# Performance work log

Hardware: AMD Instinct MI355X
Metric: run time of the kernel (lower is better)

The kernel has to match this reference:

```python
import jax, jax.numpy as jnp
import numpy as np

N = 50000        # num_nodes
E = 1_600_000    # num_edges
C = 64           # out_channels
P = 10           # periods (window_size)


def _glorot(k, shape):
    lim = np.sqrt(6.0 / (shape[0] + shape[1]))
    return jax.random.uniform(k, shape, jnp.float32, -lim, lim)


def setup_inputs() -> dict:
    key = jax.random.key(0)
    ks = jax.random.split(key, 12)
    x = jax.random.normal(ks[0], (N, 1, P), jnp.float32)
    edge_index = jax.random.randint(ks[1], (2, E), 0, N, dtype=jnp.int64)
    inp = {
        "x": x,
        "edge_index": edge_index,
        # GCNConv weights/biases for the 3 gates (in_channels=1 -> C)
        "w_cz": _glorot(ks[2], (1, C)), "b_cz": jnp.zeros((C,), jnp.float32),
        "w_cr": _glorot(ks[3], (1, C)), "b_cr": jnp.zeros((C,), jnp.float32),
        "w_ch": _glorot(ks[4], (1, C)), "b_ch": jnp.zeros((C,), jnp.float32),
        # GRU gate linears: Linear(2C -> C), stored as [in, out]
        "w_lz": _glorot(ks[5], (2 * C, C)), "b_lz": jnp.zeros((C,), jnp.float32),
        "w_lr": _glorot(ks[6], (2 * C, C)), "b_lr": jnp.zeros((C,), jnp.float32),
        "w_lh": _glorot(ks[7], (2 * C, C)), "b_lh": jnp.zeros((C,), jnp.float32),
        # temporal attention logits over periods
        "attention": jax.random.uniform(ks[8], (P,), jnp.float32),
        # output head Linear(C -> 1)
        "w_out": _glorot(ks[9], (C, 1)), "b_out": jnp.zeros((1,), jnp.float32),
    }
    return inp


def reference(x, edge_index, w_cz, b_cz, w_cr, b_cr, w_ch, b_ch,
              w_lz, b_lz, w_lr, b_lr, w_lh, b_lh, attention, w_out, b_out):
    # --- GCN symmetric normalization with self-loops (computed once) ---
    row, col = edge_index[0], edge_index[1]
    loop = jnp.arange(N, dtype=row.dtype)
    row_f = jnp.concatenate([row, loop])
    col_f = jnp.concatenate([col, loop])
    ones = jnp.ones(E + N, jnp.float32)
    deg = jax.ops.segment_sum(ones, col_f, num_segments=N)
    dinv = jnp.where(deg > 0, jax.lax.rsqrt(deg), 0.0)
    norm = dinv[row_f] * dinv[col_f]                       # [E+N]

    def gcn(xt, W, b):
        # xt: [N,1] -> lin -> propagate D^-1/2 (A+I) D^-1/2 -> + bias
        h = xt @ W                                          # [N,C]
        msg = h[row_f] * norm[:, None]                      # [E+N,C]
        return jax.ops.segment_sum(msg, col_f, num_segments=N) + b

    probs = jax.nn.softmax(attention)                       # [P]
    xs = jnp.transpose(x, (2, 0, 1))                        # [P,N,1]

    def step(carry, inp):
        H, Hacc = carry
        xt, p = inp
        Z = jax.nn.sigmoid(jnp.concatenate([gcn(xt, w_cz, b_cz), H], 1) @ w_lz + b_lz)
        R = jax.nn.sigmoid(jnp.concatenate([gcn(xt, w_cr, b_cr), H], 1) @ w_lr + b_lr)
        Ht = jnp.tanh(jnp.concatenate([gcn(xt, w_ch, b_ch), H * R], 1) @ w_lh + b_lh)
        Hn = Z * H + (1.0 - Z) * Ht
        return (Hn, Hacc + p * Hn), None

    H0 = jnp.zeros((N, C), jnp.float32)
    (_, Hacc), _ = jax.lax.scan(step, (H0, H0), (xs, probs))

    out = jnp.maximum(Hacc, 0.0) @ w_out + b_out            # ReLU + Linear(C->1)
    return out.squeeze(-1)                                   # [N]
```

## Files before the change

### kernel.cpp

```cpp
#include <hip/hip_runtime.h>
#include <math.h>


#define PT 10
#define PS 12
#define CC 64
#define CAP 96

__global__ void k_zero(unsigned int* p, int n) {
  int i = blockIdx.x * 256 + threadIdx.x;
  if (i < n) p[i] = 0u;
}

__global__ void k_deg(const int* __restrict__ col, unsigned int* deg, int E) {
  int e = blockIdx.x * 256 + threadIdx.x;
  if (e < E) atomicAdd(&deg[col[e]], 1u);
}

__global__ void k_scan1(const unsigned int* __restrict__ deg, unsigned int* rowstart,
                        unsigned int* blocksum, int n) {
  __shared__ unsigned int tmp[256];
  int i = blockIdx.x * 256 + threadIdx.x;
  unsigned int v = (i < n) ? deg[i] : 0u;
  tmp[threadIdx.x] = v;
  __syncthreads();
  for (int off = 1; off < 256; off <<= 1) {
    unsigned int t = (threadIdx.x >= off) ? tmp[threadIdx.x - off] : 0u;
    __syncthreads();
    tmp[threadIdx.x] += t;
    __syncthreads();
  }
  if (i < n) rowstart[i] = tmp[threadIdx.x] - v;
  if (threadIdx.x == 255) blocksum[blockIdx.x] = tmp[255];
}

__global__ void k_scan2(unsigned int* bs, int nb) {
  __shared__ unsigned int tmp[256];
  unsigned int v = (threadIdx.x < nb) ? bs[threadIdx.x] : 0u;
  tmp[threadIdx.x] = v;
  __syncthreads();
  for (int off = 1; off < 256; off <<= 1) {
    unsigned int t = (threadIdx.x >= off) ? tmp[threadIdx.x - off] : 0u;
    __syncthreads();
    tmp[threadIdx.x] += t;
    __syncthreads();
  }
  if (threadIdx.x < nb) bs[threadIdx.x] = tmp[threadIdx.x] - v;
}

__global__ void k_scan3(unsigned int* rowstart, const unsigned int* __restrict__ bs,
                        unsigned int* cursor, int n) {
  int i = blockIdx.x * 256 + threadIdx.x;
  if (i < n) {
    unsigned int v = rowstart[i] + bs[blockIdx.x];
    rowstart[i] = v;
    cursor[i] = v;
  }
}

__global__ void k_dinv_y(const unsigned int* __restrict__ deg, const float* __restrict__ x,
                         float* __restrict__ dinv, float* __restrict__ y, int n) {
  int v = blockIdx.x * 256 + threadIdx.x;
  if (v >= n) return;
  float di = rsqrtf((float)(deg[v] + 1u));
  dinv[v] = di;
  float* yr = y + (size_t)v * PS;
  const float* xr = x + (size_t)v * PT;
#pragma unroll
  for (int t = 0; t < PT; ++t) yr[t] = di * xr[t];
  yr[10] = 0.0f;
  yr[11] = 0.0f;
}

__global__ void k_scatter(const int* __restrict__ row, const int* __restrict__ col,
                          unsigned int* cnt_or_cursor, unsigned int* __restrict__ csr,
                          int E, int cap) {
  int e = blockIdx.x * 256 + threadIdx.x;
  if (e >= E) return;
  int c = col[e];
  unsigned int slot = atomicAdd(&cnt_or_cursor[c], 1u);
  if (cap > 0) {
    if (slot < (unsigned int)cap) csr[(size_t)c * cap + slot] = (unsigned int)row[e];
  } else {
    csr[slot] = (unsigned int)row[e];
  }
}

__global__ __launch_bounds__(256) void k_gather(
    const unsigned int* __restrict__ csr, const unsigned int* __restrict__ starts,
    const unsigned int* __restrict__ counts, const float* __restrict__ y,
    const float* __restrict__ dinv, float* __restrict__ s, int n, int cap) {
  int tid = blockIdx.x * 256 + threadIdx.x;
  int v = tid >> 2, l = tid & 3;
  if (v >= n) return;
  unsigned int cnt = counts[v];
  unsigned int start;
  if (cap > 0) {
    start = (unsigned int)v * (unsigned int)cap;
    if (cnt > (unsigned int)cap) cnt = (unsigned int)cap;
  } else {
    start = starts[v];
  }
  float a[PS];
#pragma unroll
  for (int t = 0; t < PS; ++t) a[t] = 0.0f;
  unsigned int end = start + cnt;
  for (unsigned int e = start + (unsigned int)l; e < end; e += 4u) {
    unsigned int r = csr[e];
    const float4* yr = (const float4*)(y + (size_t)r * PS);
    float4 b0 = yr[0], b1 = yr[1], b2 = yr[2];
    a[0] += b0.x; a[1] += b0.y; a[2] += b0.z; a[3] += b0.w;
    a[4] += b1.x; a[5] += b1.y; a[6] += b1.z; a[7] += b1.w;
    a[8] += b2.x; a[9] += b2.y; a[10] += b2.z; a[11] += b2.w;
  }
#pragma unroll
  for (int m = 1; m < 4; m <<= 1) {
#pragma unroll
    for (int t = 0; t < PS; ++t) a[t] += __shfl_xor(a[t], m, 64);
  }
  if (l == 0) {
    float di = dinv[v];
    const float4* ys = (const float4*)(y + (size_t)v * PS);
    float4 b0 = ys[0], b1 = ys[1], b2 = ys[2];
    float4 o0, o1, o2;
    o0.x = di * (a[0] + b0.x); o0.y = di * (a[1] + b0.y);
    o0.z = di * (a[2] + b0.z); o0.w = di * (a[3] + b0.w);
    o1.x = di * (a[4] + b1.x); o1.y = di * (a[5] + b1.y);
    o1.z = di * (a[6] + b1.z); o1.w = di * (a[7] + b1.w);
    o2.x = di * (a[8] + b2.x); o2.y = di * (a[9] + b2.y);
    o2.z = di * (a[10] + b2.z); o2.w = di * (a[11] + b2.w);
    float4* sv = (float4*)(s + (size_t)v * PS);
    sv[0] = o0; sv[1] = o1; sv[2] = o2;
  }
}

__global__ void k_sinit_fb(const float* __restrict__ y, const float* __restrict__ dinv,
                           float* __restrict__ s, int n) {
  int v = blockIdx.x * 256 + threadIdx.x;
  if (v >= n) return;
  float di = dinv[v];
#pragma unroll
  for (int t = 0; t < PS; ++t) s[(size_t)v * PS + t] = di * y[(size_t)v * PS + t];
}

__global__ void k_edge_fb(const int* __restrict__ row, const int* __restrict__ col,
                          const float* __restrict__ dinv, const float* __restrict__ y,
                          float* __restrict__ s, int E) {
  int e = blockIdx.x * 256 + threadIdx.x;
  if (e >= E) return;
  int r = row[e], c = col[e];
  float dc = dinv[c];
  const float* yr = y + (size_t)r * PS;
  float* sc = s + (size_t)c * PS;
#pragma unroll
  for (int t = 0; t < PT; ++t) atomicAdd(&sc[t], dc * yr[t]);
}

__global__ void k_prep(const float* wcz, const float* bcz, const float* wcr, const float* bcr,
                       const float* wch, const float* bch,
                       const float* wlz, const float* blz, const float* wlr, const float* blr,
                       const float* wlh, const float* blh, float* coef) {
  int c = threadIdx.x;
  float az = 0, ar = 0, ah = 0, bz = 0, br = 0, bh = 0;
  for (int m = 0; m < CC; ++m) {
    float z = wlz[m * CC + c], r = wlr[m * CC + c], h = wlh[m * CC + c];
    az += wcz[m] * z;  ar += wcr[m] * r;  ah += wch[m] * h;
    bz += bcz[m] * z;  br += bcr[m] * r;  bh += bch[m] * h;
  }
  coef[0 * CC + c] = az;
  coef[1 * CC + c] = ar;
  coef[2 * CC + c] = ah;
  coef[3 * CC + c] = bz + blz[c];
  coef[4 * CC + c] = br + blr[c];
  coef[5 * CC + c] = bh + blh[c];
}

__device__ __forceinline__ float sigf(float v) { return 1.0f / (1.0f + __expf(-v)); }
__device__ __forceinline__ float tanhfastf(float v) { return 2.0f / (1.0f + __expf(-2.0f * v)) - 1.0f; }

__device__ __forceinline__ int swz(int r, int ch) { return (ch ^ ((r >> 2) & 7)) << 2; }

__global__ __launch_bounds__(256, 4) void k_gru(
    const float* __restrict__ s, const float* __restrict__ coef,
    const float* __restrict__ wlz, const float* __restrict__ wlr, const float* __restrict__ wlh,
    const float* __restrict__ attention, const float* __restrict__ w_out,
    const float* __restrict__ b_out, float* __restrict__ out, int n) {
  __shared__ float HT[64][64];
  __shared__ float QT[64][64];
  __shared__ float sT[64][12];

  const int tid = threadIdx.x;
  const int i = tid >> 5;
  const int j = tid & 31;
  const int n0 = blockIdx.x * 64;

  for (int idx = tid; idx < 64 * 64; idx += 256) ((float*)HT)[idx] = 0.0f;
  for (int idx = tid; idx < 64 * PT; idx += 256) {
    int nn = idx / PT, t = idx - nn * PT;
    int g = n0 + nn;
    sT[nn][t] = (g < n) ? s[(size_t)g * PS + t] : 0.0f;
  }

  float att[PT];
#pragma unroll
  for (int t = 0; t < PT; ++t) att[t] = attention[t];
  float mx = att[0];
#pragma unroll
  for (int t = 1; t < PT; ++t) mx = fmaxf(mx, att[t]);
  float ssum = 0.0f;
#pragma unroll
  for (int t = 0; t < PT; ++t) { att[t] = __expf(att[t] - mx); ssum += att[t]; }
  float sinv = 1.0f / ssum;
#pragma unroll
  for (int t = 0; t < PT; ++t) att[t] *= sinv;

  const int c2 = 2 * j;
  const float2 aZ = *(const float2*)(coef + 0 + c2);
  const float2 aR = *(const float2*)(coef + 64 + c2);
  const float2 aH = *(const float2*)(coef + 128 + c2);
  const float2 bZ = *(const float2*)(coef + 192 + c2);
  const float2 bR = *(const float2*)(coef + 256 + c2);
  const float2 bH = *(const float2*)(coef + 320 + c2);
  const float* WZ = wlz + 64 * CC + c2;
  const float* WR = wlr + 64 * CC + c2;
  const float* WH = wlh + 64 * CC + c2;
  const float2 wo2 = *(const float2*)(w_out + c2);

  float hacc[8][2];
#pragma unroll
  for (int nn = 0; nn < 8; ++nn) { hacc[nn][0] = 0.0f; hacc[nn][1] = 0.0f; }

  __syncthreads();

  for (int t = 0; t < PT; ++t) {
    float sloc[8];
#pragma unroll
    for (int nn = 0; nn < 8; ++nn) sloc[nn] = sT[8 * i + nn][t];

    float acc[8][4];
#pragma unroll
    for (int nn = 0; nn < 8; ++nn) {
      acc[nn][0] = fmaf(sloc[nn], aZ.x, bZ.x);
      acc[nn][1] = fmaf(sloc[nn], aZ.y, bZ.y);
      acc[nn][2] = fmaf(sloc[nn], aR.x, bR.x);
      acc[nn][3] = fmaf(sloc[nn], aR.y, bR.y);
    }
#pragma unroll 4
    for (int k = 0; k < 64; ++k) {
      const float2 wz = *(const float2*)(WZ + (k << 6));
      const float2 wr = *(const float2*)(WR + (k << 6));
      const float4 h0 = *(const float4*)&HT[k][swz(k, 2 * i)];
      const float4 h1 = *(const float4*)&HT[k][swz(k, 2 * i + 1)];
      const float hh[8] = {h0.x, h0.y, h0.z, h0.w, h1.x, h1.y, h1.z, h1.w};
#pragma unroll
      for (int nn = 0; nn < 8; ++nn) {
        acc[nn][0] = fmaf(hh[nn], wz.x, acc[nn][0]);
        acc[nn][1] = fmaf(hh[nn], wz.y, acc[nn][1]);
        acc[nn][2] = fmaf(hh[nn], wr.x, acc[nn][2]);
        acc[nn][3] = fmaf(hh[nn], wr.y, acc[nn][3]);
      }
    }

    float hold[2][8], zreg[2][8];
#pragma unroll
    for (int cc = 0; cc < 2; ++cc) {
      int r = c2 + cc;
      float4 h0 = *(const float4*)&HT[r][swz(r, 2 * i)];
      float4 h1 = *(const float4*)&HT[r][swz(r, 2 * i + 1)];
      hold[cc][0] = h0.x; hold[cc][1] = h0.y; hold[cc][2] = h0.z; hold[cc][3] = h0.w;
      hold[cc][4] = h1.x; hold[cc][5] = h1.y; hold[cc][6] = h1.z; hold[cc][7] = h1.w;
      float4 q0, q1;
      q0.x = hold[cc][0] * sigf(acc[0][2 + cc]); q0.y = hold[cc][1] * sigf(acc[1][2 + cc]);
      q0.z = hold[cc][2] * sigf(acc[2][2 + cc]); q0.w = hold[cc][3] * sigf(acc[3][2 + cc]);
      q1.x = hold[cc][4] * sigf(acc[4][2 + cc]); q1.y = hold[cc][5] * sigf(acc[5][2 + cc]);
      q1.z = hold[cc][6] * sigf(acc[6][2 + cc]); q1.w = hold[cc][7] * sigf(acc[7][2 + cc]);
      *(float4*)&QT[r][swz(r, 2 * i)] = q0;
      *(float4*)&QT[r][swz(r, 2 * i + 1)] = q1;
#pragma unroll
      for (int nn = 0; nn < 8; ++nn) zreg[cc][nn] = sigf(acc[nn][cc]);
    }
    __syncthreads();

    float acc2[8][2];
#pragma unroll
    for (int nn = 0; nn < 8; ++nn) {
      acc2[nn][0] = fmaf(sloc[nn], aH.x, bH.x);
      acc2[nn][1] = fmaf(sloc[nn], aH.y, bH.y);
    }
#pragma unroll 4
    for (int k = 0; k < 64; ++k) {
      const float2 wv = *(const float2*)(WH + (k << 6));
      const float4 q0 = *(const float4*)&QT[k][swz(k, 2 * i)];
      const float4 q1 = *(const float4*)&QT[k][swz(k, 2 * i + 1)];
      const float qq[8] = {q0.x, q0.y, q0.z, q0.w, q1.x, q1.y, q1.z, q1.w};
#pragma unroll
      for (int nn = 0; nn < 8; ++nn) {
        acc2[nn][0] = fmaf(qq[nn], wv.x, acc2[nn][0]);
        acc2[nn][1] = fmaf(qq[nn], wv.y, acc2[nn][1]);
      }
    }

#pragma unroll
    for (int cc = 0; cc < 2; ++cc) {
      int r = c2 + cc;
      float hn[8];
#pragma unroll
      for (int nn = 0; nn < 8; ++nn) {
        float ht = tanhfastf(acc2[nn][cc]);
        float z = zreg[cc][nn];
        float v = z * hold[cc][nn] + (1.0f - z) * ht;
        hn[nn] = v;
        hacc[nn][cc] = fmaf(att[t], v, hacc[nn][cc]);
      }
      float4 v0 = make_float4(hn[0], hn[1], hn[2], hn[3]);
      float4 v1 = make_float4(hn[4], hn[5], hn[6], hn[7]);
      *(float4*)&HT[r][swz(r, 2 * i)] = v0;
      *(float4*)&HT[r][swz(r, 2 * i + 1)] = v1;
    }
    __syncthreads();
  }

  float p[8];
#pragma unroll
  for (int nn = 0; nn < 8; ++nn)
    p[nn] = fmaxf(hacc[nn][0], 0.0f) * wo2.x + fmaxf(hacc[nn][1], 0.0f) * wo2.y;
#pragma unroll
  for (int m = 1; m < 32; m <<= 1) {
#pragma unroll
    for (int nn = 0; nn < 8; ++nn) p[nn] += __shfl_xor(p[nn], m, 64);
  }
  if (j == 0) {
    float bo = b_out[0];
#pragma unroll
    for (int nn = 0; nn < 8; ++nn) {
      int g = n0 + 8 * i + nn;
      if (g < n) out[g] = p[nn] + bo;
    }
  }
}

extern "C" void kernel_launch(void* const* d_in, const int* in_sizes, int n_in,
                              void* d_out, int out_size, void* d_ws, size_t ws_size,
                              hipStream_t stream) {
  const float* x    = (const float*)d_in[0];
  const int*   ei   = (const int*)d_in[1];
  const float* wcz  = (const float*)d_in[2];
  const float* bcz  = (const float*)d_in[3];
  const float* wcr  = (const float*)d_in[4];
  const float* bcr  = (const float*)d_in[5];
  const float* wch  = (const float*)d_in[6];
  const float* bch  = (const float*)d_in[7];
  const float* wlz  = (const float*)d_in[8];
  const float* blz  = (const float*)d_in[9];
  const float* wlr  = (const float*)d_in[10];
  const float* blr  = (const float*)d_in[11];
  const float* wlh  = (const float*)d_in[12];
  const float* blh  = (const float*)d_in[13];
  const float* att  = (const float*)d_in[14];
  const float* wout = (const float*)d_in[15];
  const float* bout = (const float*)d_in[16];
  float* out = (float*)d_out;

  const int N = out_size;
  const int E = in_sizes[1] / 2;
  const int* row = ei;
  const int* col = ei + E;

  char* ws = (char*)d_ws;
  size_t off = 0;
  auto alloc = [&](size_t bytes) {
    char* p = ws + off;
    off += (bytes + 15) & ~15ull;
    return p;
  };
  unsigned int* cnt  = (unsigned int*)alloc((size_t)N * 4);
  float*        dinv = (float*)alloc((size_t)N * 4);
  float*        y    = (float*)alloc((size_t)N * PS * 4);
  float*        s    = (float*)alloc((size_t)N * PS * 4);
  float*        coef = (float*)alloc(384 * 4);
  size_t commonEnd = off;

  const size_t needA = commonEnd + (size_t)N * CAP * 4;
  const size_t needB = commonEnd + (size_t)N * 8 + 256 * 4 + (size_t)E * 4 + 64;

  const int nbN = (N + 255) / 256;
  const int nbE = (E + 255) / 256;

  k_prep<<<1, 64, 0, stream>>>(wcz, bcz, wcr, bcr, wch, bch, wlz, blz, wlr, blr, wlh, blh, coef);

  if (ws_size >= needA) {
    unsigned int* csr = (unsigned int*)(ws + commonEnd);
    k_zero<<<nbN, 256, 0, stream>>>(cnt, N);
    k_scatter<<<nbE, 256, 0, stream>>>(row, col, cnt, csr, E, CAP);
    k_dinv_y<<<nbN, 256, 0, stream>>>(cnt, x, dinv, y, N);
    k_gather<<<(4 * N + 255) / 256, 256, 0, stream>>>(csr, nullptr, cnt, y, dinv, s, N, CAP);
  } else if (ws_size >= needB) {
    size_t o = commonEnd;
    unsigned int* rowstart = (unsigned int*)(ws + o); o += (size_t)N * 4;
    unsigned int* cursor   = (unsigned int*)(ws + o); o += (size_t)N * 4;
    unsigned int* blocksum = (unsigned int*)(ws + o); o += 256 * 4;
    unsigned int* csr      = (unsigned int*)(ws + o);
    k_zero<<<nbN, 256, 0, stream>>>(cnt, N);
    k_deg<<<nbE, 256, 0, stream>>>(col, cnt, E);
    k_scan1<<<nbN, 256, 0, stream>>>(cnt, rowstart, blocksum, N);
    k_scan2<<<1, 256, 0, stream>>>(blocksum, nbN);
    k_scan3<<<nbN, 256, 0, stream>>>(rowstart, blocksum, cursor, N);
    k_dinv_y<<<nbN, 256, 0, stream>>>(cnt, x, dinv, y, N);
    k_scatter<<<nbE, 256, 0, stream>>>(row, col, cursor, csr, E, 0);
    k_gather<<<(4 * N + 255) / 256, 256, 0, stream>>>(csr, rowstart, cnt, y, dinv, s, N, 0);
  } else {
    k_zero<<<nbN, 256, 0, stream>>>(cnt, N);
    k_deg<<<nbE, 256, 0, stream>>>(col, cnt, E);
    k_dinv_y<<<nbN, 256, 0, stream>>>(cnt, x, dinv, y, N);
    k_sinit_fb<<<nbN, 256, 0, stream>>>(y, dinv, s, N);
    k_edge_fb<<<nbE, 256, 0, stream>>>(row, col, dinv, y, s, E);
  }

  k_gru<<<(N + 63) / 64, 256, 0, stream>>>(s, coef, wlz, wlr, wlh, att, wout, bout, out, N);
}
```

Before: 551.5 us.

## Halve GRU node tile to 32 and pack Z/R weights into float4

The GRU kernel now processes 32 nodes per block instead of 64, with half-size shared tiles, fewer accumulators per thread, a new swizzle, and launch bounds raised to 8 blocks per SM for higher occupancy and more blocks. The prep kernel also interleaves the hidden-part Z and R weight columns into a float4 array so each k step needs one vector global load instead of two. The trade-off is that every weight load is now reused across only 4 nodes instead of 8, which doubles total weight traffic and the number of loop iterations per node.

```diff
diff --git a/kernel.cpp b/kernel.cpp
--- a/kernel.cpp
+++ b/kernel.cpp
@@ -5,6 +5,7 @@
 #define PT 10
 #define PS 12
 #define CC 64
+#define NB 32
 #define CAP 96
 
 __global__ void k_zero(unsigned int* p, int n) {
@@ -159,43 +160,52 @@
 __global__ void k_prep(const float* wcz, const float* bcz, const float* wcr, const float* bcr,
                        const float* wch, const float* bch,
                        const float* wlz, const float* blz, const float* wlr, const float* blr,
-                       const float* wlh, const float* blh, float* coef) {
-  int c = threadIdx.x;
-  float az = 0, ar = 0, ah = 0, bz = 0, br = 0, bh = 0;
-  for (int m = 0; m < CC; ++m) {
-    float z = wlz[m * CC + c], r = wlr[m * CC + c], h = wlh[m * CC + c];
-    az += wcz[m] * z;  ar += wcr[m] * r;  ah += wch[m] * h;
-    bz += bcz[m] * z;  br += bcr[m] * r;  bh += bch[m] * h;
-  }
-  coef[0 * CC + c] = az;
-  coef[1 * CC + c] = ar;
-  coef[2 * CC + c] = ah;
-  coef[3 * CC + c] = bz + blz[c];
-  coef[4 * CC + c] = br + blr[c];
-  coef[5 * CC + c] = bh + blh[c];
+                       const float* wlh, const float* blh, float* coef, float4* packZR) {
+  int tid = threadIdx.x;
+  if (tid < 64) {
+    int c = tid;
+    float az = 0, ar = 0, ah = 0, bz = 0, br = 0, bh = 0;
+    for (int m = 0; m < CC; ++m) {
+      float z = wlz[m * CC + c], r = wlr[m * CC + c], h = wlh[m * CC + c];
+      az += wcz[m] * z;  ar += wcr[m] * r;  ah += wch[m] * h;
+      bz += bcz[m] * z;  br += bcr[m] * r;  bh += bch[m] * h;
+    }
+    coef[0 * CC + c] = az;
+    coef[1 * CC + c] = ar;
+    coef[2 * CC + c] = ah;
+    coef[3 * CC + c] = bz + blz[c];
+    coef[4 * CC + c] = br + blr[c];
+    coef[5 * CC + c] = bh + blh[c];
+  }
+  for (int idx = tid; idx < 64 * 32; idx += 256) {
+    int k = idx >> 5, j = idx & 31;
+    const float* z = wlz + (64 + k) * CC + 2 * j;
+    const float* r = wlr + (64 + k) * CC + 2 * j;
+    packZR[idx] = make_float4(z[0], z[1], r[0], r[1]);
+  }
 }
 
 __device__ __forceinline__ float sigf(float v) { return 1.0f / (1.0f + __expf(-v)); }
 __device__ __forceinline__ float tanhfastf(float v) { return 2.0f / (1.0f + __expf(-2.0f * v)) - 1.0f; }
 
-__device__ __forceinline__ int swz(int r, int ch) { return (ch ^ ((r >> 2) & 7)) << 2; }
-
-__global__ __launch_bounds__(256, 4) void k_gru(
+__device__ __forceinline__ int sc(int r, int g) { return ((g ^ ((r >> 1) & 7)) << 2); }
+
+__global__ __launch_bounds__(256, 8) void k_gru(
     const float* __restrict__ s, const float* __restrict__ coef,
-    const float* __restrict__ wlz, const float* __restrict__ wlr, const float* __restrict__ wlh,
+    const float4* __restrict__ packZR, const float* __restrict__ wlh,
     const float* __restrict__ attention, const float* __restrict__ w_out,
     const float* __restrict__ b_out, float* __restrict__ out, int n) {
-  __shared__ float HT[64][64];
-  __shared__ float QT[64][64];
-  __shared__ float sT[64][12];
+  __shared__ float HT[64][32];
+  __shared__ float QT[64][32];
+  __shared__ float sT[NB][PT];
 
   const int tid = threadIdx.x;
   const int i = tid >> 5;
   const int j = tid & 31;
-  const int n0 = blockIdx.x * 64;
-
-  for (int idx = tid; idx < 64 * 64; idx += 256) ((float*)HT)[idx] = 0.0f;
-  for (int idx = tid; idx < 64 * PT; idx += 256) {
+  const int n0 = blockIdx.x * NB;
+
+  for (int idx = tid; idx < 64 * 32; idx += 256) ((float*)HT)[idx] = 0.0f;
+  for (int idx = tid; idx < NB * PT; idx += 256) {
     int nn = idx / PT, t = idx - nn * PT;
     int g = n0 + nn;
     sT[nn][t] = (g < n) ? s[(size_t)g * PS + t] : 0.0f;
@@ -221,80 +231,71 @@
   const float2 bZ = *(const float2*)(coef + 192 + c2);
   const float2 bR = *(const float2*)(coef + 256 + c2);
   const float2 bH = *(const float2*)(coef + 320 + c2);
-  const float* WZ = wlz + 64 * CC + c2;
-  const float* WR = wlr + 64 * CC + c2;
   const float* WH = wlh + 64 * CC + c2;
+  const float4* PZ = packZR + j;
   const float2 wo2 = *(const float2*)(w_out + c2);
 
-  float hacc[8][2];
-#pragma unroll
-  for (int nn = 0; nn < 8; ++nn) { hacc[nn][0] = 0.0f; hacc[nn][1] = 0.0f; }
+  float hacc[4][2];
+#pragma unroll
+  for (int nn = 0; nn < 4; ++nn) { hacc[nn][0] = 0.0f; hacc[nn][1] = 0.0f; }
 
   __syncthreads();
 
   for (int t = 0; t < PT; ++t) {
-    float sloc[8];
-#pragma unroll
-    for (int nn = 0; nn < 8; ++nn) sloc[nn] = sT[8 * i + nn][t];
-
-    float acc[8][4];
-#pragma unroll
-    for (int nn = 0; nn < 8; ++nn) {
+    float sloc[4];
+#pragma unroll
+    for (int nn = 0; nn < 4; ++nn) sloc[nn] = sT[4 * i + nn][t];
+
+    float acc[4][4];
+#pragma unroll
+    for (int nn = 0; nn < 4; ++nn) {
       acc[nn][0] = fmaf(sloc[nn], aZ.x, bZ.x);
       acc[nn][1] = fmaf(sloc[nn], aZ.y, bZ.y);
       acc[nn][2] = fmaf(sloc[nn], aR.x, bR.x);
       acc[nn][3] = fmaf(sloc[nn], aR.y, bR.y);
     }
-#pragma unroll 4
+#pragma unroll 8
     for (int k = 0; k < 64; ++k) {
-      const float2 wz = *(const float2*)(WZ + (k << 6));
-      const float2 wr = *(const float2*)(WR + (k << 6));
-      const float4 h0 = *(const float4*)&HT[k][swz(k, 2 * i)];
-      const float4 h1 = *(const float4*)&HT[k][swz(k, 2 * i + 1)];
-      const float hh[8] = {h0.x, h0.y, h0.z, h0.w, h1.x, h1.y, h1.z, h1.w};
-#pragma unroll
-      for (int nn = 0; nn < 8; ++nn) {
-        acc[nn][0] = fmaf(hh[nn], wz.x, acc[nn][0]);
-        acc[nn][1] = fmaf(hh[nn], wz.y, acc[nn][1]);
-        acc[nn][2] = fmaf(hh[nn], wr.x, acc[nn][2]);
-        acc[nn][3] = fmaf(hh[nn], wr.y, acc[nn][3]);
+      const float4 wv = PZ[k << 5];
+      const float4 h = *(const float4*)&HT[k][sc(k, i)];
+      const float hh[4] = {h.x, h.y, h.z, h.w};
+#pragma unroll
+      for (int nn = 0; nn < 4; ++nn) {
+        acc[nn][0] = fmaf(hh[nn], wv.x, acc[nn][0]);
+        acc[nn][1] = fmaf(hh[nn], wv.y, acc[nn][1]);
+        acc[nn][2] = fmaf(hh[nn], wv.z, acc[nn][2]);
+        acc[nn][3] = fmaf(hh[nn], wv.w, acc[nn][3]);
       }
     }
 
-    float hold[2][8], zreg[2][8];
+    float hold[2][4], zreg[2][4];
 #pragma unroll
     for (int cc = 0; cc < 2; ++cc) {
       int r = c2 + cc;
-      float4 h0 = *(const float4*)&HT[r][swz(r, 2 * i)];
-      float4 h1 = *(const float4*)&HT[r][swz(r, 2 * i + 1)];
-      hold[cc][0] = h0.x; hold[cc][1] = h0.y; hold[cc][2] = h0.z; hold[cc][3] = h0.w;
-      hold[cc][4] = h1.x; hold[cc][5] = h1.y; hold[cc][6] = h1.z; hold[cc][7] = h1.w;
-      float4 q0, q1;
-      q0.x = hold[cc][0] * sigf(acc[0][2 + cc]); q0.y = hold[cc][1] * sigf(acc[1][2 + cc]);
-      q0.z = hold[cc][2] * sigf(acc[2][2 + cc]); q0.w = hold[cc][3] * sigf(acc[3][2 + cc]);
-      q1.x = hold[cc][4] * sigf(acc[4][2 + cc]); q1.y = hold[cc][5] * sigf(acc[5][2 + cc]);
-      q1.z = hold[cc][6] * sigf(acc[6][2 + cc]); q1.w = hold[cc][7] * sigf(acc[7][2 + cc]);
-      *(float4*)&QT[r][swz(r, 2 * i)] = q0;
-      *(float4*)&QT[r][swz(r, 2 * i + 1)] = q1;
-#pragma unroll
-      for (int nn = 0; nn < 8; ++nn) zreg[cc][nn] = sigf(acc[nn][cc]);
-    }
-    __syncthreads();
-
-    float acc2[8][2];
-#pragma unroll
-    for (int nn = 0; nn < 8; ++nn) {
+      float4 h = *(const float4*)&HT[r][sc(r, i)];
+      hold[cc][0] = h.x; hold[cc][1] = h.y; hold[cc][2] = h.z; hold[cc][3] = h.w;
+      float4 q;
+      q.x = h.x * sigf(acc[0][2 + cc]); q.y = h.y * sigf(acc[1][2 + cc]);
+      q.z = h.z * sigf(acc[2][2 + cc]); q.w = h.w * sigf(acc[3][2 + cc]);
+      *(float4*)&QT[r][sc(r, i)] = q;
+#pragma unroll
+      for (int nn = 0; nn < 4; ++nn) zreg[cc][nn] = sigf(acc[nn][cc]);
+    }
+    __syncthreads();
+
+    float acc2[4][2];
+#pragma unroll
+    for (int nn = 0; nn < 4; ++nn) {
       acc2[nn][0] = fmaf(sloc[nn], aH.x, bH.x);
       acc2[nn][1] = fmaf(sloc[nn], aH.y, bH.y);
     }
-#pragma unroll 4
+#pragma unroll 8
     for (int k = 0; k < 64; ++k) {
       const float2 wv = *(const float2*)(WH + (k << 6));
-      const float4 q0 = *(const float4*)&QT[k][swz(k, 2 * i)];
-      const float4 q1 = *(const float4*)&QT[k][swz(k, 2 * i + 1)];
-      const float qq[8] = {q0.x, q0.y, q0.z, q0.w, q1.x, q1.y, q1.z, q1.w};
-#pragma unroll
-      for (int nn = 0; nn < 8; ++nn) {
+      const float4 q = *(const float4*)&QT[k][sc(k, i)];
+      const float qq[4] = {q.x, q.y, q.z, q.w};
+#pragma unroll
+      for (int nn = 0; nn < 4; ++nn) {
         acc2[nn][0] = fmaf(qq[nn], wv.x, acc2[nn][0]);
         acc2[nn][1] = fmaf(qq[nn], wv.y, acc2[nn][1]);
       }
@@ -303,37 +304,34 @@
 #pragma unroll
     for (int cc = 0; cc < 2; ++cc) {
       int r = c2 + cc;
-      float hn[8];
-#pragma unroll
-      for (int nn = 0; nn < 8; ++nn) {
+      float hn[4];
+#pragma unroll
+      for (int nn = 0; nn < 4; ++nn) {
         float ht = tanhfastf(acc2[nn][cc]);
         float z = zreg[cc][nn];
         float v = z * hold[cc][nn] + (1.0f - z) * ht;
         hn[nn] = v;
         hacc[nn][cc] = fmaf(att[t], v, hacc[nn][cc]);
       }
-      float4 v0 = make_float4(hn[0], hn[1], hn[2], hn[3]);
-      float4 v1 = make_float4(hn[4], hn[5], hn[6], hn[7]);
-      *(float4*)&HT[r][swz(r, 2 * i)] = v0;
-      *(float4*)&HT[r][swz(r, 2 * i + 1)] = v1;
-    }
-    __syncthreads();
-  }
-
-  float p[8];
-#pragma unroll
-  for (int nn = 0; nn < 8; ++nn)
+      *(float4*)&HT[r][sc(r, i)] = make_float4(hn[0], hn[1], hn[2], hn[3]);
+    }
+    __syncthreads();
+  }
+
+  float p[4];
+#pragma unroll
+  for (int nn = 0; nn < 4; ++nn)
     p[nn] = fmaxf(hacc[nn][0], 0.0f) * wo2.x + fmaxf(hacc[nn][1], 0.0f) * wo2.y;
 #pragma unroll
   for (int m = 1; m < 32; m <<= 1) {
 #pragma unroll
-    for (int nn = 0; nn < 8; ++nn) p[nn] += __shfl_xor(p[nn], m, 64);
+    for (int nn = 0; nn < 4; ++nn) p[nn] += __shfl_xor(p[nn], m, 64);
   }
   if (j == 0) {
     float bo = b_out[0];
 #pragma unroll
-    for (int nn = 0; nn < 8; ++nn) {
-      int g = n0 + 8 * i + nn;
+    for (int nn = 0; nn < 4; ++nn) {
+      int g = n0 + 4 * i + nn;
       if (g < n) out[g] = p[nn] + bo;
     }
   }
@@ -378,6 +376,7 @@
   float*        y    = (float*)alloc((size_t)N * PS * 4);
   float*        s    = (float*)alloc((size_t)N * PS * 4);
   float*        coef = (float*)alloc(384 * 4);
+  float4*       packZR = (float4*)alloc(64 * 32 * 16);
   size_t commonEnd = off;
 
   const size_t needA = commonEnd + (size_t)N * CAP * 4;
@@ -386,7 +385,8 @@
   const int nbN = (N + 255) / 256;
   const int nbE = (E + 255) / 256;
 
-  k_prep<<<1, 64, 0, stream>>>(wcz, bcz, wcr, bcr, wch, bch, wlz, blz, wlr, blr, wlh, blh, coef);
+  k_prep<<<1, 256, 0, stream>>>(wcz, bcz, wcr, bcr, wch, bch, wlz, blz, wlr, blr,
+                                wlh, blh, coef, packZR);
 
   if (ws_size >= needA) {
     unsigned int* csr = (unsigned int*)(ws + commonEnd);
@@ -416,5 +416,5 @@
     k_edge_fb<<<nbE, 256, 0, stream>>>(row, col, dinv, y, s, E);
   }
 
-  k_gru<<<(N + 63) / 64, 256, 0, stream>>>(s, coef, wlz, wlr, wlh, att, wout, bout, out, N);
-}
+  k_gru<<<(N + NB - 1) / NB, 256, 0, stream>>>(s, coef, packZR, wlh, att, wout, bout, out, N);
+}
```

New measurement: 598.5 us. +8.5%, slower.
